# Optimization experiments

Measured on AMD Instinct MI355X. Metric: run time of the kernel, lower is better.

The kernel has to match this reference:

```python
import jax, jax.numpy as jnp
import numpy as np

N, D, E, H, O, TOP_K = 16384, 1024, 8, 2048, 1024, 2
LN_EPS = 1e-5


def _layernorm(h, g, b):
    # h: [E, N, F]; g, b: [E, 1, F]
    mu = h.mean(axis=-1, keepdims=True)
    var = ((h - mu) ** 2).mean(axis=-1, keepdims=True)
    return (h - mu) * jax.lax.rsqrt(var + LN_EPS) * g + b


def setup_inputs() -> dict:
    key = jax.random.key(0)
    ks = jax.random.split(key, 16)
    s = lambda fan_in: 1.0 / np.sqrt(fan_in)
    return {
        "x": jax.random.normal(ks[0], (N, D), dtype=jnp.float32),
        "Wg1": jax.random.uniform(ks[1], (D, 2 * E), jnp.float32, -s(D), s(D)),
        "Wg2": jax.random.uniform(ks[2], (2 * E, E), jnp.float32, -s(2 * E), s(2 * E)),
        "W1": jax.random.uniform(ks[3], (E, D, H), jnp.float32, -s(D), s(D)),
        "b1": jax.random.uniform(ks[4], (E, H), jnp.float32, -s(D), s(D)),
        "g1": jnp.ones((E, H), jnp.float32),
        "be1": jnp.zeros((E, H), jnp.float32),
        "W2": jax.random.uniform(ks[5], (E, H, H), jnp.float32, -s(H), s(H)),
        "b2": jax.random.uniform(ks[6], (E, H), jnp.float32, -s(H), s(H)),
        "g2": jnp.ones((E, H), jnp.float32),
        "be2": jnp.zeros((E, H), jnp.float32),
        "W3": jax.random.uniform(ks[7], (E, H, O), jnp.float32, -s(H), s(H)),
        "b3": jax.random.uniform(ks[8], (E, O), jnp.float32, -s(H), s(H)),
    }


def reference(x, Wg1, Wg2, W1, b1, g1, be1, W2, b2, g2, be2, W3, b3):
    # Gate: Linear(no bias) -> tanh -> Linear(no bias) -> softmax -> top-k
    gate_logits = jnp.tanh(x @ Wg1) @ Wg2                      # [N, E]
    gate_w = jax.nn.softmax(gate_logits, axis=-1)
    topk_w, topk_i = jax.lax.top_k(gate_w, TOP_K)              # [N, K]
    topk_w = topk_w / (topk_w.sum(axis=-1, keepdims=True) + 1e-12)
    # Dense combine weights [N, E] (equals sum over k of routed weight)
    n_idx = jnp.arange(x.shape[0])[:, None]
    cw = jnp.zeros(gate_w.shape, dtype=x.dtype).at[n_idx, topk_i].add(topk_w)
    # Expert MLPs run densely on all tokens (same math as masked dispatch;
    # unselected experts get combine weight 0). Dropout is identity (eval).
    h = jnp.einsum("nd,edh->enh", x, W1) + b1[:, None, :]
    h = jax.nn.gelu(_layernorm(h, g1[:, None, :], be1[:, None, :]), approximate=False)
    h = jnp.einsum("enh,ehk->enk", h, W2) + b2[:, None, :]
    h = jax.nn.gelu(_layernorm(h, g2[:, None, :], be2[:, None, :]), approximate=False)
    y = jnp.einsum("enh,eho->eno", h, W3) + b3[:, None, :]    # [E, N, O]
    return jnp.einsum("eno,ne->no", y, cw)                     # [N, O]
```

## Files before the change

kernel.cpp:

```cpp
#include <hip/hip_runtime.h>
#include <math.h>
#include <stdint.h>

#define N_TOK 16384
#define DIM   1024
#define NEXP  8
#define HID   2048
#define OUTD  1024
#define PADTOT 34816

typedef __attribute__((ext_vector_type(8))) short short8;
typedef __attribute__((ext_vector_type(8))) _Float16 f16x8;
typedef __attribute__((ext_vector_type(4))) float f32x4;
typedef __attribute__((ext_vector_type(4))) unsigned short u16x4;

__device__ __forceinline__ unsigned short f2h(float f) {
  return __builtin_bit_cast(unsigned short, (_Float16)f);
}
__device__ __forceinline__ float h2f(unsigned short h) {
  return (float)__builtin_bit_cast(_Float16, h);
}
__device__ __forceinline__ float gelu_exact(float a) {
  return 0.5f * a * (1.0f + erff(a * 0.70710678118654752f));
}

__global__ __launch_bounds__(256) void wg1t_kernel(
    const float* __restrict__ Wg1, float* __restrict__ Wg1t)
{
  const int t = blockIdx.x * 256 + threadIdx.x;
  const int d0 = t >> 4, j = t & 15;
  f32x4 v;
#pragma unroll
  for (int c = 0; c < 4; ++c) v[c] = Wg1[(size_t)(d0 * 4 + c) * 16 + j];
  *(f32x4*)(Wg1t + (size_t)d0 * 64 + j * 4) = v;
}

__global__ __launch_bounds__(256) void gate_kernel(
    const float* __restrict__ x, const float* __restrict__ Wg1t,
    const float* __restrict__ Wg2,
    int* __restrict__ tok_e, float* __restrict__ tok_w)
{
  const int tid = threadIdx.x;
  const int lane = tid & 63, wid = tid >> 6;
  const int j = lane & 15, g4 = lane >> 4;
  for (int tk = 0; tk < 2; ++tk) {
    const int n = blockIdx.x * 8 + wid * 2 + tk;
    const float* xrow = x + (size_t)n * DIM;
    double acc = 0.0;
    for (int it = 0; it < DIM / 16; ++it) {
      f32x4 xq = *(const f32x4*)(xrow + it * 16 + g4 * 4);
      f32x4 wq = *(const f32x4*)(Wg1t + ((size_t)it * 4 + g4) * 64 + j * 4);
#pragma unroll
      for (int c = 0; c < 4; ++c)
        acc += (double)xq[c] * (double)wq[c];
    }
    acc += __shfl_xor(acc, 16);
    acc += __shfl_xor(acc, 32);
    double t = tanh(acc);
    const int e = lane & 7;
    double ge = 0.0;
#pragma unroll
    for (int jj = 0; jj < 16; ++jj) {
      double tj = __shfl(t, jj);
      ge += tj * (double)Wg2[jj * 8 + e];
    }
    double m = ge;
#pragma unroll
    for (int s = 1; s < 8; s <<= 1) m = fmax(m, __shfl_xor(m, s));
    double p = exp(ge - m);
    double ssum = p;
#pragma unroll
    for (int s = 1; s < 8; s <<= 1) ssum += __shfl_xor(ssum, s);
    double wsm = p / ssum;
    unsigned long long key =
        (((unsigned long long)__double_as_longlong(wsm)) & ~7ULL) |
        (unsigned long long)(7 - e);
    unsigned long long k1 = key;
#pragma unroll
    for (int s = 1; s < 8; s <<= 1) { unsigned long long o = __shfl_xor(k1, s); k1 = (o > k1) ? o : k1; }
    int e1 = 7 - (int)(k1 & 7ULL);
    unsigned long long k2 = (e == e1) ? 0ULL : key;
#pragma unroll
    for (int s = 1; s < 8; s <<= 1) { unsigned long long o = __shfl_xor(k2, s); k2 = (o > k2) ? o : k2; }
    int e2 = 7 - (int)(k2 & 7ULL);
    double w1v = __longlong_as_double((long long)(k1 & ~7ULL));
    double w2v = __longlong_as_double((long long)(k2 & ~7ULL));
    double inv = 1.0 / (w1v + w2v + 1e-12);
    if (lane == 0) {
      tok_e[2 * n] = e1; tok_e[2 * n + 1] = e2;
      tok_w[2 * n] = (float)(w1v * inv); tok_w[2 * n + 1] = (float)(w2v * inv);
    }
  }
}

__global__ __launch_bounds__(256) void hist_kernel(
    const int* __restrict__ tok_e, int* __restrict__ cnt)
{
  __shared__ int h[NEXP];
  const int tid = threadIdx.x;
  if (tid < NEXP) h[tid] = 0;
  __syncthreads();
  const int base = blockIdx.x * 512;
  atomicAdd(&h[tok_e[base + tid]], 1);
  atomicAdd(&h[tok_e[base + 256 + tid]], 1);
  __syncthreads();
  if (tid < NEXP) atomicAdd(&cnt[tid], h[tid]);
}

__global__ void offsets_kernel(const int* __restrict__ cnt, int* __restrict__ off,
                               int* __restrict__ cur) {
  if (threadIdx.x == 0) {
    int a = 0;
    for (int e = 0; e < NEXP; ++e) {
      off[e] = a; cur[e] = a;
      a += (cnt[e] + 255) & ~255;
    }
    off[NEXP] = a;
  }
}

__global__ __launch_bounds__(256) void scatter_kernel(
    const int* __restrict__ tok_e, const float* __restrict__ tok_w,
    int* __restrict__ cur, int* __restrict__ rows, float* __restrict__ roww,
    int* __restrict__ pair)
{
  __shared__ int lcnt[NEXP];
  __shared__ int lbase[NEXP];
  const int tid = threadIdx.x;
  if (tid < NEXP) lcnt[tid] = 0;
  __syncthreads();
  const int n = blockIdx.x * 256 + tid;
  const int e0 = tok_e[2 * n], e1 = tok_e[2 * n + 1];
  const int r0 = atomicAdd(&lcnt[e0], 1);
  const int r1 = atomicAdd(&lcnt[e1], 1);
  __syncthreads();
  if (tid < NEXP) lbase[tid] = atomicAdd(&cur[tid], lcnt[tid]);
  __syncthreads();
  const int p0 = lbase[e0] + r0;
  const int p1 = lbase[e1] + r1;
  rows[p0] = n; roww[p0] = tok_w[2 * n];     pair[2 * n]     = p0;
  rows[p1] = n; roww[p1] = tok_w[2 * n + 1]; pair[2 * n + 1] = p1;
}

__global__ __launch_bounds__(256) void convert_x_kernel(
    const float* __restrict__ x, unsigned short* __restrict__ xh)
{
  size_t i = ((size_t)blockIdx.x * 256 + threadIdx.x) * 8;
  f32x4 a = *(const f32x4*)(x + i);
  f32x4 b = *(const f32x4*)(x + i + 4);
  short8 o;
#pragma unroll
  for (int q = 0; q < 4; ++q) { o[q] = (short)f2h(a[q]); o[q + 4] = (short)f2h(b[q]); }
  *(short8*)(xh + i) = o;
}

__global__ __launch_bounds__(256) void wconv_kernel(
    const float* __restrict__ W, unsigned short* __restrict__ Wt,
    const int K, const int N)
{
  __shared__ float t[64][65];
  const int e = blockIdx.z;
  const float* We = W + (size_t)e * K * N;
  unsigned short* Wte = Wt + (size_t)e * K * N;
  const int n0 = blockIdx.x * 64, k0 = blockIdx.y * 64;
  const int tid = threadIdx.x;
  const int rr0 = tid >> 4, c4 = (tid & 15) * 4;
#pragma unroll
  for (int rr = 0; rr < 4; ++rr) {
    const int r = rr * 16 + rr0;
    f32x4 v = *(const f32x4*)(We + (size_t)(k0 + r) * N + n0 + c4);
    t[r][c4 + 0] = v[0]; t[r][c4 + 1] = v[1]; t[r][c4 + 2] = v[2]; t[r][c4 + 3] = v[3];
  }
  __syncthreads();
#pragma unroll
  for (int rr = 0; rr < 4; ++rr) {
    const int nn = rr * 16 + rr0;
    u16x4 o;
#pragma unroll
    for (int q = 0; q < 4; ++q) o[q] = f2h(t[c4 + q][nn]);
    *(u16x4*)(Wte + (size_t)(n0 + nn) * K + k0 + c4) = o;
  }
}


#define STAGEA(SB_, T_) do {                                                  \
  _Pragma("unroll") for (int qm_ = 0; qm_ < 2; ++qm_)                         \
  _Pragma("unroll") for (int i_ = 0; i_ < 2; ++i_)                            \
    __builtin_amdgcn_global_load_lds(                                         \
      (const __attribute__((address_space(1))) void*)(Abase + aoff[qm_][i_] + (size_t)(T_)*64 + kc8), \
      (__attribute__((address_space(3))) void*)(lds + (SB_)*16384 + qm_*4096 + i_*8192 + tid*8), \
      16, 0, 0);                                                              \
} while (0)

#define STAGEB(SB_, T_) do {                                                  \
  _Pragma("unroll") for (int qn_ = 0; qn_ < 2; ++qn_)                         \
  _Pragma("unroll") for (int i_ = 0; i_ < 2; ++i_)                            \
    __builtin_amdgcn_global_load_lds(                                         \
      (const __attribute__((address_space(1))) void*)(Bbase + boff[qn_][i_] + (size_t)(T_)*64 + kc8), \
      (__attribute__((address_space(3))) void*)(lds + 32768 + (SB_)*16384 + qn_*2048 + (i_*2 + (tid >> 8))*4096 + (tid & 255)*8), \
      16, 0, 0);                                                              \
} while (0)

#define LOAD_AF(QM_) do {                                                     \
    _Pragma("unroll") for (int mi = 0; mi < 4; ++mi)                          \
    _Pragma("unroll") for (int kk = 0; kk < 2; ++kk) {                        \
      const int row_ = wm*128 + (QM_)*64 + mi*16 + l15;                       \
      const int ch_ = ((kk*4 + lh) ^ (row_ & 7));                             \
      af[mi][kk] = *(const short8*)(ldsAb + row_*64 + ch_*8);                 \
    }                                                                         \
} while (0)

#define LOAD_BF() do {                                                        \
    _Pragma("unroll") for (int qn = 0; qn < 2; ++qn)                          \
    _Pragma("unroll") for (int ni = 0; ni < 2; ++ni)                          \
    _Pragma("unroll") for (int kk = 0; kk < 2; ++kk) {                        \
      const int row_ = wn*64 + qn*32 + ni*16 + l15;                           \
      const int ch_ = ((kk*4 + lh) ^ (row_ & 7));                             \
      bf[qn][ni][kk] = *(const short8*)(ldsBb + row_*64 + ch_*8);             \
    }                                                                         \
} while (0)

#define MFMA_HALF(QM_) do {                                                   \
    __builtin_amdgcn_s_setprio(1);                                            \
    _Pragma("unroll") for (int kk = 0; kk < 2; ++kk)                          \
    _Pragma("unroll") for (int mi = 0; mi < 4; ++mi)                          \
    _Pragma("unroll") for (int qn = 0; qn < 2; ++qn)                          \
    _Pragma("unroll") for (int ni = 0; ni < 2; ++ni)                          \
      acc[(QM_)*4 + mi][qn*2 + ni] = __builtin_amdgcn_mfma_f32_16x16x32_f16(  \
          __builtin_bit_cast(f16x8, bf[qn][ni][kk]),                          \
          __builtin_bit_cast(f16x8, af[mi][kk]),                              \
          acc[(QM_)*4 + mi][qn*2 + ni], 0, 0, 0);                             \
    __builtin_amdgcn_s_setprio(0);                                            \
} while (0)

#define SYNC_LGKM_BAR() do {                                                  \
  asm volatile("s_waitcnt lgkmcnt(0)" ::: "memory");                          \
  asm volatile("s_barrier" ::: "memory");                                     \
} while (0)
#define PH_END(N_) do {                                                       \
  asm volatile("s_waitcnt vmcnt(" #N_ ") lgkmcnt(0)" ::: "memory");           \
  asm volatile("s_barrier" ::: "memory");                                     \
} while (0)

template<int MODE>
__global__ __launch_bounds__(512, 1) void gemm256_kernel(
    const unsigned short* __restrict__ Abase,
    const unsigned short* __restrict__ Bbase,
    unsigned short* __restrict__ Oh,
    float* __restrict__ Of,
    const float* __restrict__ bias,
    const int* __restrict__ rows,
    const float* __restrict__ roww,
    const int* __restrict__ off,
    const int K, const int N, const int Astride, const int c0, const int lgGX)
{
  const unsigned orig = blockIdx.x, nwg = gridDim.x;
  const unsigned q8 = nwg >> 3, r8 = nwg & 7;
  const unsigned xcd = orig & 7, pos = orig >> 3;
  const unsigned wrk = (xcd < r8 ? xcd * (q8 + 1) : r8 * (q8 + 1) + (xcd - r8) * q8) + pos;
  const int tn = (int)(wrk & ((1u << lgGX) - 1u));
  const int rowbase = c0 + (int)(wrk >> lgGX) * 256;

  const int off8 = off[NEXP];
  if (rowbase >= off8) return;
  int e = 0;
  while (e < NEXP - 1 && rowbase >= off[e + 1]) ++e;

  __shared__ __align__(16) unsigned short lds[65536];

  const int tid = threadIdx.x, lane = tid & 63, wid = tid >> 6;
  const int wm = wid >> 2, wn = wid & 3;
  const int l15 = lane & 15, lh = lane >> 4;
  const int kc8 = ((tid & 7) ^ ((tid >> 3) & 7)) * 8;

  f32x4 acc[8][4] = {};

  size_t aoff[2][2];
#pragma unroll
  for (int qm = 0; qm < 2; ++qm)
#pragma unroll
    for (int i = 0; i < 2; ++i) {
      int grow = rowbase + i * 128 + qm * 64 + (tid >> 3);
      size_t arow = (MODE == 0) ? (size_t)rows[grow] : (size_t)(grow - c0);
      aoff[qm][i] = arow * (size_t)Astride;
    }
  size_t boff[2][2];
#pragma unroll
  for (int qn = 0; qn < 2; ++qn)
#pragma unroll
    for (int i = 0; i < 2; ++i) {
      int rl = i * 64 + (tid >> 3);
      int brow = (rl >> 5) * 64 + qn * 32 + (rl & 31);
      boff[qn][i] = ((size_t)e * N + (size_t)(tn * 256 + brow)) * (size_t)K;
    }

  const int nt = K >> 6;
  STAGEA(0, 0); STAGEB(0, 0); STAGEB(1, 1);
  PH_END(4);

  for (int t = 0; t < nt; ++t) {
    const int b = t & 1;
    const unsigned short* ldsAb = lds + b * 16384;
    const unsigned short* ldsBb = lds + 32768 + b * 16384;
    short8 af[4][2], bf[2][2][2];
    if (t + 1 < nt) STAGEA(b ^ 1, t + 1);
    LOAD_AF(0); LOAD_BF();
    MFMA_HALF(0);
    SYNC_LGKM_BAR();
    if (t + 2 < nt) STAGEB(b, t + 2);
    LOAD_AF(1);
    MFMA_HALF(1);
    if (t + 2 < nt) PH_END(4); else PH_END(0);
  }

  if (MODE == 2) {
#pragma unroll
    for (int mi = 0; mi < 8; ++mi) {
      int g = rowbase + wm * 128 + mi * 16 + l15;
      int token = rows[g];
      float wgt = roww[g];
#pragma unroll
      for (int ni = 0; ni < 4; ++ni) {
        int n = tn * 256 + wn * 64 + ni * 16 + lh * 4;
        f32x4 v = acc[mi][ni];
        f32x4 bv = *(const f32x4*)(bias + (size_t)e * N + n);
#pragma unroll
        for (int qd = 0; qd < 4; ++qd)
          atomicAdd(&Of[(size_t)token * N + n + qd], wgt * (v[qd] + bv[qd]));
      }
    }
    return;
  }

  __syncthreads();
#pragma unroll
  for (int mi = 0; mi < 8; ++mi) {
    const int row = wm * 128 + mi * 16 + l15;
    float wgt = 1.0f;
    if (MODE == 3) wgt = roww[rowbase + row];
#pragma unroll
    for (int ni = 0; ni < 4; ++ni) {
      const int col = wn * 64 + ni * 16 + lh * 4;
      f32x4 v = acc[mi][ni];
      f32x4 bv = *(const f32x4*)(bias + (size_t)e * N + tn * 256 + col);
      u16x4 h;
#pragma unroll
      for (int qd = 0; qd < 4; ++qd) {
        float vv = v[qd] + bv[qd];
        if (MODE == 3) vv *= wgt;
        h[qd] = f2h(vv);
      }
      const int ch = (col >> 3) ^ (row & 7);
      *(u16x4*)(lds + row * 256 + ch * 8 + (col & 7)) = h;
    }
  }
  __syncthreads();
#pragma unroll
  for (int it = 0; it < 16; ++it) {
    const int flat = it * 512 + tid;
    const int row = flat >> 5;
    const int ch = flat & 31;
    const int chs = ch ^ (row & 7);
    short8 v = *(const short8*)(lds + row * 256 + chs * 8);
    const int g = rowbase + row;
    unsigned short* dst = (MODE == 3) ? (Oh + (size_t)g * N)
                                      : (Oh + (size_t)(g - c0) * N);
    *(short8*)(dst + tn * 256 + ch * 8) = v;
  }
}

__global__ __launch_bounds__(256) void ln_gelu_kernel(
    const unsigned short* __restrict__ src, unsigned short* __restrict__ dst,
    const float* __restrict__ gam, const float* __restrict__ bet,
    const int* __restrict__ off, const int c0)
{
  const int wid = threadIdx.x >> 6, lane = threadIdx.x & 63;
  const int g = c0 + blockIdx.x * 4 + wid;
  if (g >= off[NEXP]) return;
  int e = 0;
#pragma unroll
  for (int q = 1; q < NEXP; ++q) if (g >= off[q]) e = q;
  const unsigned short* s0 = src + (size_t)(g - c0) * HID;
  float v[32];
  float s = 0.f, sq = 0.f;
#pragma unroll
  for (int ch = 0; ch < 4; ++ch) {
    short8 hv = *(const short8*)(s0 + ch * 512 + lane * 8);
#pragma unroll
    for (int q = 0; q < 8; ++q) {
      float f = h2f((unsigned short)hv[q]);
      v[ch * 8 + q] = f;
      s += f; sq += f * f;
    }
  }
#pragma unroll
  for (int sh = 32; sh > 0; sh >>= 1) { s += __shfl_xor(s, sh); sq += __shfl_xor(sq, sh); }
  const float mu  = s * (1.0f / HID);
  const float var = sq * (1.0f / HID) - mu * mu;
  const float rstd = rsqrtf(var + 1e-5f);
  const float* ge_ = gam + (size_t)e * HID;
  const float* be_ = bet + (size_t)e * HID;
  unsigned short* d0 = dst + (size_t)(g - c0) * HID;
#pragma unroll
  for (int ch = 0; ch < 4; ++ch) {
    const int base = ch * 512 + lane * 8;
    f32x4 ga = *(const f32x4*)(ge_ + base);
    f32x4 gb = *(const f32x4*)(ge_ + base + 4);
    f32x4 ba = *(const f32x4*)(be_ + base);
    f32x4 bb = *(const f32x4*)(be_ + base + 4);
    short8 o;
#pragma unroll
    for (int q = 0; q < 4; ++q) {
      float t1 = (v[ch * 8 + q] - mu) * rstd * ga[q] + ba[q];
      float t2 = (v[ch * 8 + 4 + q] - mu) * rstd * gb[q] + bb[q];
      o[q] = (short)f2h(gelu_exact(t1));
      o[q + 4] = (short)f2h(gelu_exact(t2));
    }
    *(short8*)(d0 + base) = o;
  }
}

__global__ __launch_bounds__(256) void combine_kernel(
    const unsigned short* __restrict__ Y, const int* __restrict__ pair,
    float* __restrict__ out)
{
  const int n = blockIdx.x;
  const int j = threadIdx.x * 4;
  const int r1 = pair[2 * n], r2 = pair[2 * n + 1];
  u16x4 a = *(const u16x4*)(Y + (size_t)r1 * OUTD + j);
  u16x4 b = *(const u16x4*)(Y + (size_t)r2 * OUTD + j);
  f32x4 o;
#pragma unroll
  for (int qd = 0; qd < 4; ++qd) o[qd] = h2f(a[qd]) + h2f(b[qd]);
  *(f32x4*)(out + (size_t)n * OUTD + j) = o;
}

__global__ void probe_kernel(float* out, float v) {
  if (threadIdx.x == 0 && blockIdx.x == 0) out[0] = v;
}

extern "C" void kernel_launch(void* const* d_in, const int* in_sizes, int n_in,
                              void* d_out, int out_size, void* d_ws, size_t ws_size,
                              hipStream_t stream) {
  (void)in_sizes; (void)n_in;
  const float* x   = (const float*)d_in[0];
  const float* Wg1 = (const float*)d_in[1];
  const float* Wg2 = (const float*)d_in[2];
  const float* W1  = (const float*)d_in[3];
  const float* b1  = (const float*)d_in[4];
  const float* g1  = (const float*)d_in[5];
  const float* be1 = (const float*)d_in[6];
  const float* W2  = (const float*)d_in[7];
  const float* b2  = (const float*)d_in[8];
  const float* g2  = (const float*)d_in[9];
  const float* be2 = (const float*)d_in[10];
  const float* W3  = (const float*)d_in[11];
  const float* b3  = (const float*)d_in[12];
  float* out = (float*)d_out;

  uint8_t* w = (uint8_t*)d_ws;
  auto alloc = [&](size_t bytes) {
    uint8_t* p = w;
    w += (bytes + 255) & ~(size_t)255;
    return p;
  };
  unsigned short* xh   = (unsigned short*)alloc((size_t)N_TOK * DIM * 2);
  unsigned short* Wt1  = (unsigned short*)alloc((size_t)NEXP * DIM * HID * 2);
  unsigned short* Wt2  = (unsigned short*)alloc((size_t)NEXP * HID * HID * 2);
  unsigned short* Wt3  = (unsigned short*)alloc((size_t)NEXP * HID * OUTD * 2);
  float* Wg1t  = (float*)alloc((size_t)DIM * 16 * 4);
  int*   rows  = (int*)alloc((size_t)PADTOT * 4);
  float* roww  = (float*)alloc((size_t)PADTOT * 4);
  int*   tok_e = (int*)alloc((size_t)2 * N_TOK * 4);
  float* tok_w = (float*)alloc((size_t)2 * N_TOK * 4);
  int*   pair  = (int*)alloc((size_t)2 * N_TOK * 4);
  int*   cnt   = (int*)alloc(256);
  int*   off   = (int*)alloc(256);
  int*   cur   = (int*)alloc(256);
  size_t fixed_used = (size_t)(w - (uint8_t*)d_ws);

  long long availLL = (long long)ws_size - (long long)fixed_used - 4096;
  int R = 0;
  if (availLL > 0) {
    long long r = availLL / (HID * 2 + HID * 2);
    if (r > PADTOT) r = PADTOT;
    R = (int)(r & ~255LL);
  }
  if (R < 256) {
    hipMemsetAsync(d_out, 0, (size_t)out_size * sizeof(float), stream);
    probe_kernel<<<1, 64, 0, stream>>>(out, (float)(ws_size >> 20));
    return;
  }
  unsigned short* act1h = (unsigned short*)alloc((size_t)R * HID * 2);
  unsigned short* act2  = (unsigned short*)alloc((size_t)R * HID * 2);
  const bool single = (R >= PADTOT);
  unsigned short* Yh = act1h;

  hipMemsetAsync(cnt, 0, NEXP * sizeof(int), stream);
  hipMemsetAsync(rows, 0, (size_t)PADTOT * 4, stream);
  hipMemsetAsync(roww, 0, (size_t)PADTOT * 4, stream);
  if (!single)
    hipMemsetAsync(d_out, 0, (size_t)out_size * sizeof(float), stream);

  wg1t_kernel<<<16, 256, 0, stream>>>(Wg1, Wg1t);
  gate_kernel<<<N_TOK / 8, 256, 0, stream>>>(x, Wg1t, Wg2, tok_e, tok_w);
  hist_kernel<<<2 * N_TOK / 512, 256, 0, stream>>>(tok_e, cnt);
  offsets_kernel<<<1, 64, 0, stream>>>(cnt, off, cur);
  scatter_kernel<<<N_TOK / 256, 256, 0, stream>>>(tok_e, tok_w, cur, rows, roww, pair);

  convert_x_kernel<<<(N_TOK * DIM / 8) / 256, 256, 0, stream>>>(x, xh);
  wconv_kernel<<<dim3(HID / 64, DIM / 64, NEXP), 256, 0, stream>>>(W1, Wt1, DIM, HID);
  wconv_kernel<<<dim3(HID / 64, HID / 64, NEXP), 256, 0, stream>>>(W2, Wt2, HID, HID);
  wconv_kernel<<<dim3(OUTD / 64, HID / 64, NEXP), 256, 0, stream>>>(W3, Wt3, HID, OUTD);

  for (int c0 = 0; c0 < PADTOT; c0 += R) {
    int Rc = PADTOT - c0; if (Rc > R) Rc = R;
    const int yt = Rc / 256;
    gemm256_kernel<0><<<8 * yt, 512, 0, stream>>>(xh, Wt1, act1h, nullptr, b1,
                                                  rows, roww, off, DIM, HID, DIM, c0, 3);
    ln_gelu_kernel<<<Rc / 4, 256, 0, stream>>>(act1h, act2, g1, be1, off, c0);
    gemm256_kernel<1><<<8 * yt, 512, 0, stream>>>(act2, Wt2, act1h, nullptr, b2,
                                                  rows, roww, off, HID, HID, HID, c0, 3);
    ln_gelu_kernel<<<Rc / 4, 256, 0, stream>>>(act1h, act2, g2, be2, off, c0);
    if (single)
      gemm256_kernel<3><<<4 * yt, 512, 0, stream>>>(act2, Wt3, Yh, nullptr, b3,
                                                    rows, roww, off, HID, OUTD, HID, c0, 2);
    else
      gemm256_kernel<2><<<4 * yt, 512, 0, stream>>>(act2, Wt3, nullptr, out, b3,
                                                    rows, roww, off, HID, OUTD, HID, c0, 2);
  }
  if (single)
    combine_kernel<<<N_TOK, 256, 0, stream>>>(Yh, pair, out);
}
```

Measured before the change: 1.010 ms.

## Shrink expert GEMM tile to 256x128 with K=32 steps and higher occupancy

Restructures the grouped expert GEMM from a 256x256 output tile with K-step 64 to a 256x128 tile with K-step 32. It uses a 4x2 wave layout, a new paired-row XOR swizzle and a simpler double-buffered pipeline that stages A and B together. LDS use is halved and launch bounds now request up to 4 blocks per CU, so more blocks can run at once and the grid doubles. In exchange, each block reuses data less, so global and LDS traffic per FLOP rises and there are more barriers per unit of work.

```diff
diff --git a/kernel.cpp b/kernel.cpp
--- a/kernel.cpp
+++ b/kernel.cpp
@@ -184,52 +184,44 @@
 
 
 #define STAGEA(SB_, T_) do {                                                  \
-  _Pragma("unroll") for (int qm_ = 0; qm_ < 2; ++qm_)                         \
   _Pragma("unroll") for (int i_ = 0; i_ < 2; ++i_)                            \
     __builtin_amdgcn_global_load_lds(                                         \
-      (const __attribute__((address_space(1))) void*)(Abase + aoff[qm_][i_] + (size_t)(T_)*64 + kc8), \
-      (__attribute__((address_space(3))) void*)(lds + (SB_)*16384 + qm_*4096 + i_*8192 + tid*8), \
+      (const __attribute__((address_space(1))) void*)(Abase + aoff[i_] + (size_t)(T_)*32), \
+      (__attribute__((address_space(3))) void*)(lds + (SB_)*8192 + (i_*512 + tid)*8), \
       16, 0, 0);                                                              \
 } while (0)
 
 #define STAGEB(SB_, T_) do {                                                  \
-  _Pragma("unroll") for (int qn_ = 0; qn_ < 2; ++qn_)                         \
-  _Pragma("unroll") for (int i_ = 0; i_ < 2; ++i_)                            \
     __builtin_amdgcn_global_load_lds(                                         \
-      (const __attribute__((address_space(1))) void*)(Bbase + boff[qn_][i_] + (size_t)(T_)*64 + kc8), \
-      (__attribute__((address_space(3))) void*)(lds + 32768 + (SB_)*16384 + qn_*2048 + (i_*2 + (tid >> 8))*4096 + (tid & 255)*8), \
+      (const __attribute__((address_space(1))) void*)(Bbase + boff + (size_t)(T_)*32), \
+      (__attribute__((address_space(3))) void*)(lds + 16384 + (SB_)*4096 + tid*8), \
       16, 0, 0);                                                              \
 } while (0)
 
-#define LOAD_AF(QM_) do {                                                     \
+#define LOAD_AF() do {                                                        \
+    _Pragma("unroll") for (int mi = 0; mi < 4; ++mi) {                        \
+      const int row_ = wm*64 + mi*16 + l15;                                   \
+      const int rp_ = row_ >> 1, sub_ = (row_ & 1)*4 + lh;                    \
+      af[mi] = *(const short8*)(ldsAb + rp_*64 + ((sub_ ^ (rp_ & 7)))*8);     \
+    }                                                                         \
+} while (0)
+
+#define LOAD_BF() do {                                                        \
+    _Pragma("unroll") for (int ni = 0; ni < 4; ++ni) {                        \
+      const int row_ = wn*64 + ni*16 + l15;                                   \
+      const int rp_ = row_ >> 1, sub_ = (row_ & 1)*4 + lh;                    \
+      bf[ni] = *(const short8*)(ldsBb + rp_*64 + ((sub_ ^ (rp_ & 7)))*8);     \
+    }                                                                         \
+} while (0)
+
+#define MFMA_TILE() do {                                                      \
+    __builtin_amdgcn_s_setprio(1);                                            \
     _Pragma("unroll") for (int mi = 0; mi < 4; ++mi)                          \
-    _Pragma("unroll") for (int kk = 0; kk < 2; ++kk) {                        \
-      const int row_ = wm*128 + (QM_)*64 + mi*16 + l15;                       \
-      const int ch_ = ((kk*4 + lh) ^ (row_ & 7));                             \
-      af[mi][kk] = *(const short8*)(ldsAb + row_*64 + ch_*8);                 \
-    }                                                                         \
-} while (0)
-
-#define LOAD_BF() do {                                                        \
-    _Pragma("unroll") for (int qn = 0; qn < 2; ++qn)                          \
-    _Pragma("unroll") for (int ni = 0; ni < 2; ++ni)                          \
-    _Pragma("unroll") for (int kk = 0; kk < 2; ++kk) {                        \
-      const int row_ = wn*64 + qn*32 + ni*16 + l15;                           \
-      const int ch_ = ((kk*4 + lh) ^ (row_ & 7));                             \
-      bf[qn][ni][kk] = *(const short8*)(ldsBb + row_*64 + ch_*8);             \
-    }                                                                         \
-} while (0)
-
-#define MFMA_HALF(QM_) do {                                                   \
-    __builtin_amdgcn_s_setprio(1);                                            \
-    _Pragma("unroll") for (int kk = 0; kk < 2; ++kk)                          \
-    _Pragma("unroll") for (int mi = 0; mi < 4; ++mi)                          \
-    _Pragma("unroll") for (int qn = 0; qn < 2; ++qn)                          \
-    _Pragma("unroll") for (int ni = 0; ni < 2; ++ni)                          \
-      acc[(QM_)*4 + mi][qn*2 + ni] = __builtin_amdgcn_mfma_f32_16x16x32_f16(  \
-          __builtin_bit_cast(f16x8, bf[qn][ni][kk]),                          \
-          __builtin_bit_cast(f16x8, af[mi][kk]),                              \
-          acc[(QM_)*4 + mi][qn*2 + ni], 0, 0, 0);                             \
+    _Pragma("unroll") for (int ni = 0; ni < 4; ++ni)                          \
+      acc[mi][ni] = __builtin_amdgcn_mfma_f32_16x16x32_f16(                   \
+          __builtin_bit_cast(f16x8, bf[ni]),                                  \
+          __builtin_bit_cast(f16x8, af[mi]),                                  \
+          acc[mi][ni], 0, 0, 0);                                              \
     __builtin_amdgcn_s_setprio(0);                                            \
 } while (0)
 
@@ -243,7 +235,7 @@
 } while (0)
 
 template<int MODE>
-__global__ __launch_bounds__(512, 1) void gemm256_kernel(
+__global__ __launch_bounds__(512, 4) void gemm256_kernel(
     const unsigned short* __restrict__ Abase,
     const unsigned short* __restrict__ Bbase,
     unsigned short* __restrict__ Oh,
@@ -266,62 +258,57 @@
   int e = 0;
   while (e < NEXP - 1 && rowbase >= off[e + 1]) ++e;
 
-  __shared__ __align__(16) unsigned short lds[65536];
+  __shared__ __align__(16) unsigned short lds[32768];
 
   const int tid = threadIdx.x, lane = tid & 63, wid = tid >> 6;
-  const int wm = wid >> 2, wn = wid & 3;
+  const int wm = wid >> 1, wn = wid & 1;
   const int l15 = lane & 15, lh = lane >> 4;
-  const int kc8 = ((tid & 7) ^ ((tid >> 3) & 7)) * 8;
-
-  f32x4 acc[8][4] = {};
-
-  size_t aoff[2][2];
-#pragma unroll
-  for (int qm = 0; qm < 2; ++qm)
-#pragma unroll
-    for (int i = 0; i < 2; ++i) {
-      int grow = rowbase + i * 128 + qm * 64 + (tid >> 3);
-      size_t arow = (MODE == 0) ? (size_t)rows[grow] : (size_t)(grow - c0);
-      aoff[qm][i] = arow * (size_t)Astride;
-    }
-  size_t boff[2][2];
-#pragma unroll
-  for (int qn = 0; qn < 2; ++qn)
-#pragma unroll
-    for (int i = 0; i < 2; ++i) {
-      int rl = i * 64 + (tid >> 3);
-      int brow = (rl >> 5) * 64 + qn * 32 + (rl & 31);
-      boff[qn][i] = ((size_t)e * N + (size_t)(tn * 256 + brow)) * (size_t)K;
-    }
-
-  const int nt = K >> 6;
-  STAGEA(0, 0); STAGEB(0, 0); STAGEB(1, 1);
-  PH_END(4);
+
+  f32x4 acc[4][4] = {};
+
+  size_t aoff[2];
+#pragma unroll
+  for (int i = 0; i < 2; ++i) {
+    const int c = i * 512 + tid;
+    const int rp = c >> 3, sl = (c & 7) ^ (rp & 7);
+    const int row = rp * 2 + (sl >> 2), kc = (sl & 3) * 8;
+    const int grow = rowbase + row;
+    size_t arow = (MODE == 0) ? (size_t)rows[grow] : (size_t)(grow - c0);
+    aoff[i] = arow * (size_t)Astride + kc;
+  }
+  size_t boff;
+  {
+    const int c = tid;
+    const int rp = c >> 3, sl = (c & 7) ^ (rp & 7);
+    const int brow = rp * 2 + (sl >> 2), kc = (sl & 3) * 8;
+    boff = ((size_t)e * N + (size_t)(tn * 128 + brow)) * (size_t)K + kc;
+  }
+
+  const int nt = K >> 5;
+  STAGEA(0, 0); STAGEB(0, 0); STAGEA(1, 1); STAGEB(1, 1);
+  PH_END(3);
 
   for (int t = 0; t < nt; ++t) {
     const int b = t & 1;
-    const unsigned short* ldsAb = lds + b * 16384;
-    const unsigned short* ldsBb = lds + 32768 + b * 16384;
-    short8 af[4][2], bf[2][2][2];
-    if (t + 1 < nt) STAGEA(b ^ 1, t + 1);
-    LOAD_AF(0); LOAD_BF();
-    MFMA_HALF(0);
+    const unsigned short* ldsAb = lds + b * 8192;
+    const unsigned short* ldsBb = lds + 16384 + b * 4096;
+    short8 af[4], bf[4];
+    LOAD_AF(); LOAD_BF();
     SYNC_LGKM_BAR();
-    if (t + 2 < nt) STAGEB(b, t + 2);
-    LOAD_AF(1);
-    MFMA_HALF(1);
-    if (t + 2 < nt) PH_END(4); else PH_END(0);
+    if (t + 2 < nt) { STAGEA(b, t + 2); STAGEB(b, t + 2); }
+    MFMA_TILE();
+    if (t + 2 < nt) PH_END(3); else PH_END(0);
   }
 
   if (MODE == 2) {
 #pragma unroll
-    for (int mi = 0; mi < 8; ++mi) {
-      int g = rowbase + wm * 128 + mi * 16 + l15;
+    for (int mi = 0; mi < 4; ++mi) {
+      int g = rowbase + wm * 64 + mi * 16 + l15;
       int token = rows[g];
       float wgt = roww[g];
 #pragma unroll
       for (int ni = 0; ni < 4; ++ni) {
-        int n = tn * 256 + wn * 64 + ni * 16 + lh * 4;
+        int n = tn * 128 + wn * 64 + ni * 16 + lh * 4;
         f32x4 v = acc[mi][ni];
         f32x4 bv = *(const f32x4*)(bias + (size_t)e * N + n);
 #pragma unroll
@@ -334,15 +321,15 @@
 
   __syncthreads();
 #pragma unroll
-  for (int mi = 0; mi < 8; ++mi) {
-    const int row = wm * 128 + mi * 16 + l15;
+  for (int mi = 0; mi < 4; ++mi) {
+    const int row = wm * 64 + mi * 16 + l15;
     float wgt = 1.0f;
     if (MODE == 3) wgt = roww[rowbase + row];
 #pragma unroll
     for (int ni = 0; ni < 4; ++ni) {
       const int col = wn * 64 + ni * 16 + lh * 4;
       f32x4 v = acc[mi][ni];
-      f32x4 bv = *(const f32x4*)(bias + (size_t)e * N + tn * 256 + col);
+      f32x4 bv = *(const f32x4*)(bias + (size_t)e * N + tn * 128 + col);
       u16x4 h;
 #pragma unroll
       for (int qd = 0; qd < 4; ++qd) {
@@ -350,22 +337,22 @@
         if (MODE == 3) vv *= wgt;
         h[qd] = f2h(vv);
       }
-      const int ch = (col >> 3) ^ (row & 7);
-      *(u16x4*)(lds + row * 256 + ch * 8 + (col & 7)) = h;
-    }
-  }
-  __syncthreads();
-#pragma unroll
-  for (int it = 0; it < 16; ++it) {
+      const int ch = col >> 3;
+      *(u16x4*)(lds + row * 128 + (ch ^ (row & 7)) * 8 + (col & 7)) = h;
+    }
+  }
+  __syncthreads();
+#pragma unroll
+  for (int it = 0; it < 8; ++it) {
     const int flat = it * 512 + tid;
-    const int row = flat >> 5;
-    const int ch = flat & 31;
+    const int row = flat >> 4;
+    const int ch = flat & 15;
     const int chs = ch ^ (row & 7);
-    short8 v = *(const short8*)(lds + row * 256 + chs * 8);
+    short8 v = *(const short8*)(lds + row * 128 + chs * 8);
     const int g = rowbase + row;
     unsigned short* dst = (MODE == 3) ? (Oh + (size_t)g * N)
                                       : (Oh + (size_t)(g - c0) * N);
-    *(short8*)(dst + tn * 256 + ch * 8) = v;
+    *(short8*)(dst + tn * 128 + ch * 8) = v;
   }
 }
 
@@ -516,18 +503,18 @@
   for (int c0 = 0; c0 < PADTOT; c0 += R) {
     int Rc = PADTOT - c0; if (Rc > R) Rc = R;
     const int yt = Rc / 256;
-    gemm256_kernel<0><<<8 * yt, 512, 0, stream>>>(xh, Wt1, act1h, nullptr, b1,
-                                                  rows, roww, off, DIM, HID, DIM, c0, 3);
+    gemm256_kernel<0><<<16 * yt, 512, 0, stream>>>(xh, Wt1, act1h, nullptr, b1,
+                                                   rows, roww, off, DIM, HID, DIM, c0, 4);
     ln_gelu_kernel<<<Rc / 4, 256, 0, stream>>>(act1h, act2, g1, be1, off, c0);
-    gemm256_kernel<1><<<8 * yt, 512, 0, stream>>>(act2, Wt2, act1h, nullptr, b2,
-                                                  rows, roww, off, HID, HID, HID, c0, 3);
+    gemm256_kernel<1><<<16 * yt, 512, 0, stream>>>(act2, Wt2, act1h, nullptr, b2,
+                                                   rows, roww, off, HID, HID, HID, c0, 4);
     ln_gelu_kernel<<<Rc / 4, 256, 0, stream>>>(act1h, act2, g2, be2, off, c0);
     if (single)
-      gemm256_kernel<3><<<4 * yt, 512, 0, stream>>>(act2, Wt3, Yh, nullptr, b3,
-                                                    rows, roww, off, HID, OUTD, HID, c0, 2);
+      gemm256_kernel<3><<<8 * yt, 512, 0, stream>>>(act2, Wt3, Yh, nullptr, b3,
+                                                    rows, roww, off, HID, OUTD, HID, c0, 3);
     else
-      gemm256_kernel<2><<<4 * yt, 512, 0, stream>>>(act2, Wt3, nullptr, out, b3,
-                                                    rows, roww, off, HID, OUTD, HID, c0, 2);
+      gemm256_kernel<2><<<8 * yt, 512, 0, stream>>>(act2, Wt3, nullptr, out, b3,
+                                                    rows, roww, off, HID, OUTD, HID, c0, 3);
   }
   if (single)
     combine_kernel<<<N_TOK, 256, 0, stream>>>(Yh, pair, out);
```

New measurement: 1.062 ms. 1.05x slower.

## Make expert GEMMs persistent with per-XCD atomic tile claiming

Applied to the files above, without the earlier changes.

Replaces the one-block-per-tile launch with a fixed grid of 256 persistent workgroups. Each workgroup loops, claiming tiles from a per-XCD atomic counter, and sizes the tile count from the actual routed row total, so padded empty tiles are never launched. This targets the cost of launching and retiring blocks that exit early, and aims to balance tail work across CUs. In exchange it adds a memset per chunk, atomic claims and a barrier per tile.

```diff
diff --git a/kernel.cpp b/kernel.cpp
--- a/kernel.cpp
+++ b/kernel.cpp
@@ -252,120 +252,134 @@
     const int* __restrict__ rows,
     const float* __restrict__ roww,
     const int* __restrict__ off,
-    const int K, const int N, const int Astride, const int c0, const int lgGX)
-{
-  const unsigned orig = blockIdx.x, nwg = gridDim.x;
-  const unsigned q8 = nwg >> 3, r8 = nwg & 7;
-  const unsigned xcd = orig & 7, pos = orig >> 3;
-  const unsigned wrk = (xcd < r8 ? xcd * (q8 + 1) : r8 * (q8 + 1) + (xcd - r8) * q8) + pos;
-  const int tn = (int)(wrk & ((1u << lgGX) - 1u));
-  const int rowbase = c0 + (int)(wrk >> lgGX) * 256;
-
+    int* __restrict__ tcnt,
+    const int K, const int N, const int Astride, const int c0, const int lgGX,
+    const int ntmMax)
+{
   const int off8 = off[NEXP];
-  if (rowbase >= off8) return;
-  int e = 0;
-  while (e < NEXP - 1 && rowbase >= off[e + 1]) ++e;
+  int ntm = (off8 - c0 + 255) >> 8;
+  if (ntm > ntmMax) ntm = ntmMax;
+  if (ntm <= 0) return;
+  const int total = ntm << lgGX;
+
+  const int xcd = blockIdx.x & 7;
+  const int q8 = total >> 3, r8 = total & 7;
+  const int base = (xcd < r8) ? xcd * (q8 + 1) : r8 * (q8 + 1) + (xcd - r8) * q8;
+  const int len  = (xcd < r8) ? q8 + 1 : q8;
 
   __shared__ __align__(16) unsigned short lds[65536];
+  __shared__ int sclaim;
 
   const int tid = threadIdx.x, lane = tid & 63, wid = tid >> 6;
   const int wm = wid >> 2, wn = wid & 3;
   const int l15 = lane & 15, lh = lane >> 4;
   const int kc8 = ((tid & 7) ^ ((tid >> 3) & 7)) * 8;
-
-  f32x4 acc[8][4] = {};
-
-  size_t aoff[2][2];
-#pragma unroll
-  for (int qm = 0; qm < 2; ++qm)
-#pragma unroll
-    for (int i = 0; i < 2; ++i) {
-      int grow = rowbase + i * 128 + qm * 64 + (tid >> 3);
-      size_t arow = (MODE == 0) ? (size_t)rows[grow] : (size_t)(grow - c0);
-      aoff[qm][i] = arow * (size_t)Astride;
-    }
-  size_t boff[2][2];
-#pragma unroll
-  for (int qn = 0; qn < 2; ++qn)
-#pragma unroll
-    for (int i = 0; i < 2; ++i) {
-      int rl = i * 64 + (tid >> 3);
-      int brow = (rl >> 5) * 64 + qn * 32 + (rl & 31);
-      boff[qn][i] = ((size_t)e * N + (size_t)(tn * 256 + brow)) * (size_t)K;
-    }
-
   const int nt = K >> 6;
-  STAGEA(0, 0); STAGEB(0, 0); STAGEB(1, 1);
-  PH_END(4);
-
-  for (int t = 0; t < nt; ++t) {
-    const int b = t & 1;
-    const unsigned short* ldsAb = lds + b * 16384;
-    const unsigned short* ldsBb = lds + 32768 + b * 16384;
-    short8 af[4][2], bf[2][2][2];
-    if (t + 1 < nt) STAGEA(b ^ 1, t + 1);
-    LOAD_AF(0); LOAD_BF();
-    MFMA_HALF(0);
-    SYNC_LGKM_BAR();
-    if (t + 2 < nt) STAGEB(b, t + 2);
-    LOAD_AF(1);
-    MFMA_HALF(1);
-    if (t + 2 < nt) PH_END(4); else PH_END(0);
-  }
-
-  if (MODE == 2) {
+
+  for (;;) {
+    if (tid == 0) sclaim = atomicAdd(&tcnt[xcd], 1);
+    __syncthreads();
+    const int kcl = sclaim;
+    if (kcl >= len) break;
+    const int wrk = base + kcl;
+    const int tn = wrk & ((1 << lgGX) - 1);
+    const int rowbase = c0 + (wrk >> lgGX) * 256;
+    int e = 0;
+    while (e < NEXP - 1 && rowbase >= off[e + 1]) ++e;
+
+    f32x4 acc[8][4] = {};
+
+    size_t aoff[2][2];
+#pragma unroll
+    for (int qm = 0; qm < 2; ++qm)
+#pragma unroll
+      for (int i = 0; i < 2; ++i) {
+        int grow = rowbase + i * 128 + qm * 64 + (tid >> 3);
+        size_t arow = (MODE == 0) ? (size_t)rows[grow] : (size_t)(grow - c0);
+        aoff[qm][i] = arow * (size_t)Astride;
+      }
+    size_t boff[2][2];
+#pragma unroll
+    for (int qn = 0; qn < 2; ++qn)
+#pragma unroll
+      for (int i = 0; i < 2; ++i) {
+        int rl = i * 64 + (tid >> 3);
+        int brow = (rl >> 5) * 64 + qn * 32 + (rl & 31);
+        boff[qn][i] = ((size_t)e * N + (size_t)(tn * 256 + brow)) * (size_t)K;
+      }
+
+    STAGEA(0, 0); STAGEB(0, 0); STAGEB(1, 1);
+    PH_END(4);
+
+    for (int t = 0; t < nt; ++t) {
+      const int b = t & 1;
+      const unsigned short* ldsAb = lds + b * 16384;
+      const unsigned short* ldsBb = lds + 32768 + b * 16384;
+      short8 af[4][2], bf[2][2][2];
+      if (t + 1 < nt) STAGEA(b ^ 1, t + 1);
+      LOAD_AF(0); LOAD_BF();
+      MFMA_HALF(0);
+      SYNC_LGKM_BAR();
+      if (t + 2 < nt) STAGEB(b, t + 2);
+      LOAD_AF(1);
+      MFMA_HALF(1);
+      if (t + 2 < nt) PH_END(4); else PH_END(0);
+    }
+
+    if (MODE == 2) {
+#pragma unroll
+      for (int mi = 0; mi < 8; ++mi) {
+        int g = rowbase + wm * 128 + mi * 16 + l15;
+        int token = rows[g];
+        float wgt = roww[g];
+#pragma unroll
+        for (int ni = 0; ni < 4; ++ni) {
+          int n = tn * 256 + wn * 64 + ni * 16 + lh * 4;
+          f32x4 v = acc[mi][ni];
+          f32x4 bv = *(const f32x4*)(bias + (size_t)e * N + n);
+#pragma unroll
+          for (int qd = 0; qd < 4; ++qd)
+            atomicAdd(&Of[(size_t)token * N + n + qd], wgt * (v[qd] + bv[qd]));
+        }
+      }
+      continue;
+    }
+
+    __syncthreads();
 #pragma unroll
     for (int mi = 0; mi < 8; ++mi) {
-      int g = rowbase + wm * 128 + mi * 16 + l15;
-      int token = rows[g];
-      float wgt = roww[g];
+      const int row = wm * 128 + mi * 16 + l15;
+      float wgt = 1.0f;
+      if (MODE == 3) wgt = roww[rowbase + row];
 #pragma unroll
       for (int ni = 0; ni < 4; ++ni) {
-        int n = tn * 256 + wn * 64 + ni * 16 + lh * 4;
+        const int col = wn * 64 + ni * 16 + lh * 4;
         f32x4 v = acc[mi][ni];
-        f32x4 bv = *(const f32x4*)(bias + (size_t)e * N + n);
-#pragma unroll
-        for (int qd = 0; qd < 4; ++qd)
-          atomicAdd(&Of[(size_t)token * N + n + qd], wgt * (v[qd] + bv[qd]));
+        f32x4 bv = *(const f32x4*)(bias + (size_t)e * N + tn * 256 + col);
+        u16x4 h;
+#pragma unroll
+        for (int qd = 0; qd < 4; ++qd) {
+          float vv = v[qd] + bv[qd];
+          if (MODE == 3) vv *= wgt;
+          h[qd] = f2h(vv);
+        }
+        const int ch = (col >> 3) ^ (row & 7);
+        *(u16x4*)(lds + row * 256 + ch * 8 + (col & 7)) = h;
       }
     }
-    return;
-  }
-
-  __syncthreads();
-#pragma unroll
-  for (int mi = 0; mi < 8; ++mi) {
-    const int row = wm * 128 + mi * 16 + l15;
-    float wgt = 1.0f;
-    if (MODE == 3) wgt = roww[rowbase + row];
-#pragma unroll
-    for (int ni = 0; ni < 4; ++ni) {
-      const int col = wn * 64 + ni * 16 + lh * 4;
-      f32x4 v = acc[mi][ni];
-      f32x4 bv = *(const f32x4*)(bias + (size_t)e * N + tn * 256 + col);
-      u16x4 h;
-#pragma unroll
-      for (int qd = 0; qd < 4; ++qd) {
-        float vv = v[qd] + bv[qd];
-        if (MODE == 3) vv *= wgt;
-        h[qd] = f2h(vv);
-      }
-      const int ch = (col >> 3) ^ (row & 7);
-      *(u16x4*)(lds + row * 256 + ch * 8 + (col & 7)) = h;
-    }
-  }
-  __syncthreads();
-#pragma unroll
-  for (int it = 0; it < 16; ++it) {
-    const int flat = it * 512 + tid;
-    const int row = flat >> 5;
-    const int ch = flat & 31;
-    const int chs = ch ^ (row & 7);
-    short8 v = *(const short8*)(lds + row * 256 + chs * 8);
-    const int g = rowbase + row;
-    unsigned short* dst = (MODE == 3) ? (Oh + (size_t)g * N)
-                                      : (Oh + (size_t)(g - c0) * N);
-    *(short8*)(dst + tn * 256 + ch * 8) = v;
+    __syncthreads();
+#pragma unroll
+    for (int it = 0; it < 16; ++it) {
+      const int flat = it * 512 + tid;
+      const int row = flat >> 5;
+      const int ch = flat & 31;
+      const int chs = ch ^ (row & 7);
+      short8 v = *(const short8*)(lds + row * 256 + chs * 8);
+      const int g = rowbase + row;
+      unsigned short* dst = (MODE == 3) ? (Oh + (size_t)g * N)
+                                        : (Oh + (size_t)(g - c0) * N);
+      *(short8*)(dst + tn * 256 + ch * 8) = v;
+    }
   }
 }
 
@@ -477,6 +491,7 @@
   int*   cnt   = (int*)alloc(256);
   int*   off   = (int*)alloc(256);
   int*   cur   = (int*)alloc(256);
+  int*   tcnt  = (int*)alloc(3 * 8 * 4);
   size_t fixed_used = (size_t)(w - (uint8_t*)d_ws);
 
   long long availLL = (long long)ws_size - (long long)fixed_used - 4096;
@@ -515,19 +530,24 @@
 
   for (int c0 = 0; c0 < PADTOT; c0 += R) {
     int Rc = PADTOT - c0; if (Rc > R) Rc = R;
-    const int yt = Rc / 256;
-    gemm256_kernel<0><<<8 * yt, 512, 0, stream>>>(xh, Wt1, act1h, nullptr, b1,
-                                                  rows, roww, off, DIM, HID, DIM, c0, 3);
+    const int ntmMax = Rc / 256;
+    hipMemsetAsync(tcnt, 0, 3 * 8 * sizeof(int), stream);
+    gemm256_kernel<0><<<256, 512, 0, stream>>>(xh, Wt1, act1h, nullptr, b1,
+                                               rows, roww, off, tcnt,
+                                               DIM, HID, DIM, c0, 3, ntmMax);
     ln_gelu_kernel<<<Rc / 4, 256, 0, stream>>>(act1h, act2, g1, be1, off, c0);
-    gemm256_kernel<1><<<8 * yt, 512, 0, stream>>>(act2, Wt2, act1h, nullptr, b2,
-                                                  rows, roww, off, HID, HID, HID, c0, 3);
+    gemm256_kernel<1><<<256, 512, 0, stream>>>(act2, Wt2, act1h, nullptr, b2,
+                                               rows, roww, off, tcnt + 8,
+                                               HID, HID, HID, c0, 3, ntmMax);
     ln_gelu_kernel<<<Rc / 4, 256, 0, stream>>>(act1h, act2, g2, be2, off, c0);
     if (single)
-      gemm256_kernel<3><<<4 * yt, 512, 0, stream>>>(act2, Wt3, Yh, nullptr, b3,
-                                                    rows, roww, off, HID, OUTD, HID, c0, 2);
+      gemm256_kernel<3><<<256, 512, 0, stream>>>(act2, Wt3, Yh, nullptr, b3,
+                                                 rows, roww, off, tcnt + 16,
+                                                 HID, OUTD, HID, c0, 2, ntmMax);
     else
-      gemm256_kernel<2><<<4 * yt, 512, 0, stream>>>(act2, Wt3, nullptr, out, b3,
-                                                    rows, roww, off, HID, OUTD, HID, c0, 2);
+      gemm256_kernel<2><<<256, 512, 0, stream>>>(act2, Wt3, nullptr, out, b3,
+                                                 rows, roww, off, tcnt + 16,
+                                                 HID, OUTD, HID, c0, 2, ntmMax);
   }
   if (single)
     combine_kernel<<<N_TOK, 256, 0, stream>>>(Yh, pair, out);
```

Measured after the change: 1.218 ms. 1.21x slower.
